# Performance work log

Hardware: AMD Instinct MI355X
Metric: run time of the kernel (lower is better)

## Reference

```python
import jax, jax.numpy as jnp
import numpy as np

DN = ('NCHW', 'HWIO', 'NCHW')  # NCHW data, HWIO kernels


def conv3x3(x, k, b=None):
    # 'same'-padded 3x3 conv, stride 1, NCHW layout
    y = jax.lax.conv_general_dilated(x, k, (1, 1), 'SAME', dimension_numbers=DN)
    if b is not None:
        y = y + b[None, :, None, None]
    return y


def setup_inputs() -> dict:
    B, T, C, H, W = 4, 4, 256, 30, 40
    CA = 256  # nb_filters_att (== nb_filters_out == nb_filters_in per SAM)
    key = jax.random.key(0)
    ks = jax.random.split(key, 10)
    s = 0.05  # small init scale so gates don't saturate
    x = jax.random.normal(ks[0], (B, T, C, H, W), dtype=jnp.float32)
    # attention convs
    Wa = jax.random.normal(ks[1], (3, 3, C, CA), dtype=jnp.float32) * s
    ba = jnp.zeros((CA,), dtype=jnp.float32)
    Ua = jax.random.normal(ks[2], (3, 3, C, CA), dtype=jnp.float32) * s
    bua = jnp.zeros((CA,), dtype=jnp.float32)
    # V_a has attentive_init='zero' in the original; random here for a nontrivial baseline
    Va = jax.random.normal(ks[3], (3, 3, CA, 1), dtype=jnp.float32) * s
    # gate convs: stack i,f,c,o along output channels (same math as 4 separate 3x3 convs)
    Wx = jax.random.normal(ks[4], (3, 3, C, 4 * C), dtype=jnp.float32) * s
    bx = jnp.zeros((4 * C,), dtype=jnp.float32)
    Uh = jax.random.normal(ks[5], (3, 3, C, 4 * C), dtype=jnp.float32) * s
    bh = jnp.zeros((4 * C,), dtype=jnp.float32)
    return {"x": x, "Wa": Wa, "ba": ba, "Ua": Ua, "bua": bua, "Va": Va,
            "Wx": Wx, "bx": bx, "Uh": Uh, "bh": bh}


def reference(x, Wa, ba, Ua, bua, Va, Wx, bx, Uh, bh):
    B, T, C, H, W = x.shape
    # initial h and c: sum over the time axis (K.sum(x, axis=1))
    h0 = jnp.sum(x, axis=1)
    c0 = h0

    def step(carry, xt):
        h, c = carry
        # conv-based spatial attention
        e = conv3x3(jnp.tanh(conv3x3(h, Wa, ba) + conv3x3(xt, Ua, bua)), Va)  # [B,1,H,W]
        a = jax.nn.softmax(e.reshape(B, -1), axis=-1).reshape(B, 1, H, W)
        x_tilde = xt * a  # broadcast over channels
        # fused gate convs: i | f | c | o along channel axis
        g = conv3x3(x_tilde, Wx, bx) + conv3x3(h, Uh, bh)  # [B,4C,H,W]
        gi, gf, gc, go = jnp.split(g, 4, axis=1)
        i = jax.nn.sigmoid(gi)
        f = jax.nn.sigmoid(gf)
        o = jax.nn.sigmoid(go)
        c_new = f * c + i * jnp.tanh(gc)
        h_new = o * jnp.tanh(c_new)
        return (h_new, c_new), None

    (h_last, _), _ = jax.lax.scan(step, (h0, c0), jnp.swapaxes(x, 0, 1))
    return h_last  # [B, C_out, H, W], the last RNN output
```

## Files before the change

### kernel.cpp

```cpp
#include <hip/hip_runtime.h>
#include <math.h>

#define BB 4
#define TT 4
#define CC 256
#define HH 30
#define WW 40
#define HWS (HH*WW)
#define CHW (CC*HWS)

typedef __attribute__((ext_vector_type(8))) _Float16 half8;
typedef __attribute__((ext_vector_type(4))) float f32x4;

__global__ void init_hc(const float* __restrict__ x,
                        float* __restrict__ h, float* __restrict__ c) {
    int id = blockIdx.x * 256 + threadIdx.x;
    if (id >= BB * CHW) return;
    int b = id / CHW;
    int rem = id - b * CHW;
    float s = 0.f;
#pragma unroll
    for (int t = 0; t < TT; ++t)
        s += x[((size_t)b * TT + t) * CHW + rem];
    h[id] = s;
    c[id] = s;
}

__global__ void pack_weights(const float* __restrict__ W1,
                             const float* __restrict__ W2,
                             _Float16* __restrict__ wt, int Cout) {
    int idx = blockIdx.x * 256 + threadIdx.x;
    if (idx >= 4608 * Cout) return;
    int k = idx / Cout;
    int n = idx - k * Cout;
    float v = (k < 2304) ? W1[(size_t)k * Cout + n]
                         : W2[(size_t)(k - 2304) * Cout + n];
    wt[((size_t)(k >> 3) * Cout + n) * 8 + (k & 7)] = (_Float16)v;
}

template<int NW>
__global__ __launch_bounds__(256) void conv_mfma(
    const float* __restrict__ in0, long bs0, const float* __restrict__ scale,
    const float* __restrict__ in1, long bs1,
    const _Float16* __restrict__ wt,
    const float* __restrict__ b1, const float* __restrict__ b2,
    float* __restrict__ out, int Cout)
{
    __shared__ alignas(16) _Float16 s_a[4 * 168 * 8];

    const int tid = threadIdx.x;
    const int l = tid & 63, wv = tid >> 6;
    const int q = l >> 4, r = l & 15;
    const int mb = blockIdx.x;
    const int b = mb / 15;
    const int pix0 = (mb % 15) * 80;
    const int y0 = (mb % 15) * 2;
    const int n0 = blockIdx.y * (4 * NW * 16) + wv * (NW * 16);
    const int z = blockIdx.z;

    const float* inp = z ? (in1 + (size_t)b * bs1) : (in0 + (size_t)b * bs0);
    const float* scl = z ? nullptr : scale;

    f32x4 acc[5][NW];
#pragma unroll
    for (int nt = 0; nt < NW; ++nt) {
        int co = n0 + nt * 16 + r;
        float bias = z ? 0.f : (b1[co] + b2[co]);
        f32x4 bv = {bias, bias, bias, bias};
#pragma unroll
        for (int mt = 0; mt < 5; ++mt) acc[mt][nt] = bv;
    }

    for (int ci0 = 0; ci0 < CC; ci0 += 32) {
        __syncthreads();
        for (int i = tid; i < 672; i += 256) {
            int cig = i / 168;
            int pix = i - cig * 168;
            int row = pix / 42;
            int px = pix - row * 42;
            int xx = px - 1, yy = y0 + row - 1;
            half8 hv = {0, 0, 0, 0, 0, 0, 0, 0};
            if (xx >= 0 && xx < WW && yy >= 0 && yy < HH) {
                const float* p0 = inp + (size_t)(ci0 + cig * 8) * HWS + yy * WW + xx;
                float sc = scl ? scl[(size_t)b * HWS + yy * WW + xx] : 1.f;
#pragma unroll
                for (int j = 0; j < 8; ++j)
                    hv[j] = (_Float16)(p0[(size_t)j * HWS] * sc);
            }
            *(half8*)&s_a[(cig * 168 + pix) * 8] = hv;
        }
        __syncthreads();

        const int kgb = z * 288 + (ci0 >> 3);
#pragma unroll
        for (int tap = 0; tap < 9; ++tap) {
            const int dy = tap / 3, dx = tap - dy * 3;
            const int kg = kgb + tap * 32 + q;
            half8 bf[NW];
#pragma unroll
            for (int nt = 0; nt < NW; ++nt) {
                size_t off = (size_t)kg * Cout + (n0 + nt * 16 + r);
                bf[nt] = ((const half8*)wt)[off];
            }
#pragma unroll
            for (int mt = 0; mt < 5; ++mt) {
                int p = mt * 16 + r;
                int ry = p / 40, rx = p - ry * 40;
                int hpix = (ry + dy) * 42 + rx + dx;
                half8 af = *(const half8*)&s_a[(q * 168 + hpix) * 8];
#pragma unroll
                for (int nt = 0; nt < NW; ++nt)
                    acc[mt][nt] = __builtin_amdgcn_mfma_f32_16x16x32_f16(
                        af, bf[nt], acc[mt][nt], 0, 0, 0);
            }
        }
    }

    out += (size_t)z * BB * Cout * HWS;
#pragma unroll
    for (int mt = 0; mt < 5; ++mt) {
#pragma unroll
        for (int nt = 0; nt < NW; ++nt) {
            int co = n0 + nt * 16 + r;
            int p = pix0 + mt * 16 + q * 4;
            *(f32x4*)&out[((size_t)b * Cout + co) * HWS + p] = acc[mt][nt];
        }
    }
}

__global__ void add_tanh(const float* __restrict__ a0, const float* __restrict__ a1,
                         float* __restrict__ o, int n) {
    int id = blockIdx.x * 256 + threadIdx.x;
    if (id < n) o[id] = tanhf(a0[id] + a1[id]);
}

__global__ __launch_bounds__(256) void att_e_part(
    const float* __restrict__ att, const float* __restrict__ Va,
    float* __restrict__ part)
{
    __shared__ float red[4][64];
    const int lane = threadIdx.x & 63, wv = threadIdx.x >> 6;
    const int p = blockIdx.x * 64 + lane;
    const int b = blockIdx.y, ch = blockIdx.z;
    const bool valid = (p < HWS);
    const int pc = valid ? p : 0;
    const int y = pc / WW, x = pc - (pc / WW) * WW;

    float acc = 0.f;
    if (valid) {
        const int ca0 = ch * 32 + wv * 8;
#pragma unroll
        for (int j = 0; j < 8; ++j) {
            const int ca = ca0 + j;
            const float* base = att + ((size_t)b * CC + ca) * HWS;
            const float* va = Va + ca;
#pragma unroll
            for (int dy = 0; dy < 3; ++dy) {
                int yy = y + dy - 1;
                if (yy < 0 || yy >= HH) continue;
#pragma unroll
                for (int dx = 0; dx < 3; ++dx) {
                    int xx = x + dx - 1;
                    if (xx < 0 || xx >= WW) continue;
                    acc = fmaf(base[yy * WW + xx], va[(dy * 3 + dx) * CC], acc);
                }
            }
        }
    }
    red[wv][lane] = acc;
    __syncthreads();
    if (wv == 0 && valid)
        part[((size_t)b * 8 + ch) * HWS + p] =
            red[0][lane] + red[1][lane] + red[2][lane] + red[3][lane];
}

__global__ __launch_bounds__(256) void softmax_kernel(
    const float* __restrict__ part, float* __restrict__ a)
{
    __shared__ float se[HWS];
    __shared__ float red[256];
    int b = blockIdx.x;
    int tid = threadIdx.x;

    for (int i = tid; i < HWS; i += 256) {
        float s = 0.f;
#pragma unroll
        for (int ch = 0; ch < 8; ++ch)
            s += part[((size_t)b * 8 + ch) * HWS + i];
        se[i] = s;
    }
    __syncthreads();

    float m = -1e30f;
    for (int i = tid; i < HWS; i += 256) m = fmaxf(m, se[i]);
    red[tid] = m;
    __syncthreads();
    for (int s = 128; s > 0; s >>= 1) {
        if (tid < s) red[tid] = fmaxf(red[tid], red[tid + s]);
        __syncthreads();
    }
    m = red[0];
    __syncthreads();

    float sum = 0.f;
    for (int i = tid; i < HWS; i += 256) {
        float v = expf(se[i] - m);
        se[i] = v;
        sum += v;
    }
    red[tid] = sum;
    __syncthreads();
    for (int s = 128; s > 0; s >>= 1) {
        if (tid < s) red[tid] += red[tid + s];
        __syncthreads();
    }
    float inv = 1.f / red[0];
    for (int i = tid; i < HWS; i += 256)
        a[(size_t)b * HWS + i] = se[i] * inv;
}

__global__ void gate_update(const float* __restrict__ g0, const float* __restrict__ g1,
                            float* __restrict__ c, float* __restrict__ h_out) {
    int id = blockIdx.x * 256 + threadIdx.x;
    if (id >= BB * CHW) return;
    int b = id / CHW;
    int rem = id - b * CHW;
    size_t gbase = (size_t)b * 4 * CHW + rem;
    float gi = g0[gbase] + g1[gbase];
    float gf = g0[gbase + CHW] + g1[gbase + CHW];
    float gc = g0[gbase + 2 * (size_t)CHW] + g1[gbase + 2 * (size_t)CHW];
    float go = g0[gbase + 3 * (size_t)CHW] + g1[gbase + 3 * (size_t)CHW];
    float i_ = 1.f / (1.f + expf(-gi));
    float f_ = 1.f / (1.f + expf(-gf));
    float o_ = 1.f / (1.f + expf(-go));
    float cn = f_ * c[id] + i_ * tanhf(gc);
    c[id] = cn;
    h_out[id] = o_ * tanhf(cn);
}

extern "C" void kernel_launch(void* const* d_in, const int* in_sizes, int n_in,
                              void* d_out, int out_size, void* d_ws, size_t ws_size,
                              hipStream_t stream) {
    const float* x   = (const float*)d_in[0];
    const float* Wa  = (const float*)d_in[1];
    const float* ba  = (const float*)d_in[2];
    const float* Ua  = (const float*)d_in[3];
    const float* bua = (const float*)d_in[4];
    const float* Va  = (const float*)d_in[5];
    const float* Wx  = (const float*)d_in[6];
    const float* bx  = (const float*)d_in[7];
    const float* Uh  = (const float*)d_in[8];
    const float* bh  = (const float*)d_in[9];
    float* out = (float*)d_out;

    char* wsb = (char*)d_ws;
    const size_t NCHW = (size_t)BB * CHW;
    _Float16* wtg = (_Float16*)wsb;               wsb += (size_t)4608 * 1024 * 2;
    _Float16* wta = (_Float16*)wsb;               wsb += (size_t)4608 * 256 * 2;
    float* h0   = (float*)wsb;                    wsb += NCHW * 4;
    float* h1   = (float*)wsb;                    wsb += NCHW * 4;
    float* cb   = (float*)wsb;                    wsb += NCHW * 4;
    float* att01= (float*)wsb;                    wsb += 2 * NCHW * 4;
    float* att  = (float*)wsb;                    wsb += NCHW * 4;
    float* g01  = (float*)wsb;                    wsb += 8 * NCHW * 4;
    float* part = (float*)wsb;                    wsb += (size_t)BB * 8 * HWS * 4;
    float* a    = (float*)wsb;

    pack_weights<<<dim3((4608 * 1024 + 255) / 256), dim3(256), 0, stream>>>(
        Wx, Uh, wtg, 1024);
    pack_weights<<<dim3((4608 * 256 + 255) / 256), dim3(256), 0, stream>>>(
        Wa, Ua, wta, 256);

    const int n = (int)NCHW;
    init_hc<<<dim3((n + 255) / 256), dim3(256), 0, stream>>>(x, h0, cb);

    float* hbuf[2] = {h0, h1};
    const long XT_BS = (long)TT * CHW;
    const long H_BS  = (long)CHW;

    for (int t = 0; t < TT; ++t) {
        const float* xt = x + (size_t)t * CHW;
        float* hcur = hbuf[t & 1];
        float* hnext = (t == TT - 1) ? out : hbuf[(t + 1) & 1];

        conv_mfma<1><<<dim3(60, 4, 2), dim3(256), 0, stream>>>(
            hcur, H_BS, nullptr, xt, XT_BS, wta, ba, bua, att01, 256);
        add_tanh<<<dim3((n + 255) / 256), dim3(256), 0, stream>>>(
            att01, att01 + NCHW, att, n);

        att_e_part<<<dim3(19, BB, 8), dim3(256), 0, stream>>>(att, Va, part);
        softmax_kernel<<<dim3(BB), dim3(256), 0, stream>>>(part, a);

        conv_mfma<2><<<dim3(60, 8, 2), dim3(256), 0, stream>>>(
            xt, XT_BS, a, hcur, H_BS, wtg, bx, bh, g01, 1024);

        gate_update<<<dim3((n + 255) / 256), dim3(256), 0, stream>>>(
            g01, g01 + 4 * NCHW, cb, hnext);
    }
}
```

Baseline: 658.3 us.

## Double-buffer conv staging, software-pipeline weight loads, split-K attention conv, vectorize elementwise

The MFMA conv kernel now double-buffers its shared-memory input tile. It prefetches the next channel chunk into registers while the current taps compute, and rotates weight registers so global weight loads overlap the MFMAs, with s_setprio raised around the compute. The attention conv is split over input channels, giving four partial outputs that add_tanh4 sums, so more blocks run on the small 256-output conv. init_hc, add_tanh and gate_update use float4 vector accesses. The changes add register pressure (launch bounds of 3 blocks per CU), double the shared memory, and write more partial-sum traffic in exchange for better latency hiding and parallelism.

```diff
diff --git a/kernel.cpp b/kernel.cpp
--- a/kernel.cpp
+++ b/kernel.cpp
@@ -8,6 +8,7 @@
 #define WW 40
 #define HWS (HH*WW)
 #define CHW (CC*HWS)
+#define CHW4 (CHW/4)
 
 typedef __attribute__((ext_vector_type(8))) _Float16 half8;
 typedef __attribute__((ext_vector_type(4))) float f32x4;
@@ -15,15 +16,16 @@
 __global__ void init_hc(const float* __restrict__ x,
                         float* __restrict__ h, float* __restrict__ c) {
     int id = blockIdx.x * 256 + threadIdx.x;
-    if (id >= BB * CHW) return;
-    int b = id / CHW;
-    int rem = id - b * CHW;
-    float s = 0.f;
+    if (id >= BB * CHW4) return;
+    int b = id / CHW4;
+    int rem = id - b * CHW4;
+    const f32x4* xv = (const f32x4*)x;
+    f32x4 s = {0.f, 0.f, 0.f, 0.f};
 #pragma unroll
     for (int t = 0; t < TT; ++t)
-        s += x[((size_t)b * TT + t) * CHW + rem];
-    h[id] = s;
-    c[id] = s;
+        s += xv[((size_t)b * TT + t) * CHW4 + rem];
+    ((f32x4*)h)[id] = s;
+    ((f32x4*)c)[id] = s;
 }
 
 __global__ void pack_weights(const float* __restrict__ W1,
@@ -38,15 +40,16 @@
     wt[((size_t)(k >> 3) * Cout + n) * 8 + (k & 7)] = (_Float16)v;
 }
 
-template<int NW>
-__global__ __launch_bounds__(256) void conv_mfma(
+template<int NW, int NZ>
+__global__ __launch_bounds__(256, 3) void conv_mfma(
     const float* __restrict__ in0, long bs0, const float* __restrict__ scale,
     const float* __restrict__ in1, long bs1,
     const _Float16* __restrict__ wt,
     const float* __restrict__ b1, const float* __restrict__ b2,
     float* __restrict__ out, int Cout)
 {
-    __shared__ alignas(16) _Float16 s_a[4 * 168 * 8];
+    constexpr int NK = 8 / NZ;
+    __shared__ alignas(16) _Float16 s_a[2][4 * 168 * 8];
 
     const int tid = threadIdx.x;
     const int l = tid & 63, wv = tid >> 6;
@@ -57,64 +60,124 @@
     const int y0 = (mb % 15) * 2;
     const int n0 = blockIdx.y * (4 * NW * 16) + wv * (NW * 16);
     const int z = blockIdx.z;
-
-    const float* inp = z ? (in1 + (size_t)b * bs1) : (in0 + (size_t)b * bs0);
-    const float* scl = z ? nullptr : scale;
+    const int src = z / NZ;
+    const int ci_start = (z % NZ) * (CC / NZ);
+    const int kgb0 = src * 288 + (ci_start >> 3);
+
+    const float* inp = (src ? in1 + (size_t)b * bs1 : in0 + (size_t)b * bs0)
+                       + (size_t)ci_start * HWS;
+    const float* scl = (src == 0) ? scale : nullptr;
+
+    bool iv[3], pv[3];
+    const float* pj[3];
+    float sc[3];
+    int ldsoff[3];
+#pragma unroll
+    for (int j = 0; j < 3; ++j) {
+        int item = tid + j * 256;
+        iv[j] = item < 672;
+        int it = iv[j] ? item : 0;
+        int cig = it / 168;
+        int pix = it - cig * 168;
+        int row = pix / 42;
+        int px = pix - row * 42;
+        int xx = px - 1, yy = y0 + row - 1;
+        pv[j] = iv[j] && xx >= 0 && xx < WW && yy >= 0 && yy < HH;
+        pj[j] = inp + (size_t)(cig * 8) * HWS + yy * WW + xx;
+        sc[j] = 1.f;
+        if (scl && pv[j]) sc[j] = scl[(size_t)b * HWS + yy * WW + xx];
+        ldsoff[j] = (cig * 168 + pix) * 8;
+    }
 
     f32x4 acc[5][NW];
 #pragma unroll
     for (int nt = 0; nt < NW; ++nt) {
         int co = n0 + nt * 16 + r;
-        float bias = z ? 0.f : (b1[co] + b2[co]);
+        float bias = (z == 0) ? (b1[co] + b2[co]) : 0.f;
         f32x4 bv = {bias, bias, bias, bias};
 #pragma unroll
         for (int mt = 0; mt < 5; ++mt) acc[mt][nt] = bv;
     }
 
-    for (int ci0 = 0; ci0 < CC; ci0 += 32) {
+    int hbase[5];
+#pragma unroll
+    for (int mt = 0; mt < 5; ++mt) {
+        int p = mt * 16 + r;
+        int ry = p / 40;
+        int rx = p - ry * 40;
+        hbase[mt] = ry * 42 + rx;
+    }
+
+    float sr[3][8];
+    auto stage_issue = [&](int kk) {
+#pragma unroll
+        for (int j = 0; j < 3; ++j) if (pv[j]) {
+            const float* p0 = pj[j] + (size_t)kk * 32 * HWS;
+#pragma unroll
+            for (int t = 0; t < 8; ++t) sr[j][t] = p0[(size_t)t * HWS];
+        }
+    };
+    auto stage_write = [&](int kk) {
+#pragma unroll
+        for (int j = 0; j < 3; ++j) if (iv[j]) {
+            half8 hv = {0, 0, 0, 0, 0, 0, 0, 0};
+            if (pv[j]) {
+#pragma unroll
+                for (int t = 0; t < 8; ++t)
+                    hv[t] = (_Float16)(sr[j][t] * sc[j]);
+            }
+            *(half8*)&s_a[kk & 1][ldsoff[j]] = hv;
+        }
+    };
+
+    const half8* wp = (const half8*)wt;
+    half8 w0[NW], w1[NW], w2[NW], w3[NW];
+
+#define WLOAD(SLOT, TAP) do {                                              \
+    const int kg_ = kgb0 + k * 4 + (TAP) * 32 + q;                         \
+    _Pragma("unroll")                                                      \
+    for (int nt = 0; nt < NW; ++nt)                                        \
+        SLOT[nt] = wp[(size_t)kg_ * Cout + n0 + nt * 16 + r];              \
+} while (0)
+
+#define CTAP(SLOT, TAP) do {                                               \
+    constexpr int dy_ = (TAP) / 3, dx_ = (TAP) % 3;                        \
+    _Pragma("unroll")                                                      \
+    for (int mt = 0; mt < 5; ++mt) {                                       \
+        half8 af = *(const half8*)&s_a[k & 1]                              \
+            [(q * 168 + hbase[mt] + dy_ * 42 + dx_) * 8];                  \
+        _Pragma("unroll")                                                  \
+        for (int nt = 0; nt < NW; ++nt)                                    \
+            acc[mt][nt] = __builtin_amdgcn_mfma_f32_16x16x32_f16(          \
+                af, SLOT[nt], acc[mt][nt], 0, 0, 0);                       \
+    }                                                                      \
+} while (0)
+
+    stage_issue(0);
+    stage_write(0);
+
+#pragma unroll
+    for (int k = 0; k < NK; ++k) {
+        WLOAD(w0, 0); WLOAD(w1, 1); WLOAD(w2, 2);
+        if (k + 1 < NK) stage_issue(k + 1);
         __syncthreads();
-        for (int i = tid; i < 672; i += 256) {
-            int cig = i / 168;
-            int pix = i - cig * 168;
-            int row = pix / 42;
-            int px = pix - row * 42;
-            int xx = px - 1, yy = y0 + row - 1;
-            half8 hv = {0, 0, 0, 0, 0, 0, 0, 0};
-            if (xx >= 0 && xx < WW && yy >= 0 && yy < HH) {
-                const float* p0 = inp + (size_t)(ci0 + cig * 8) * HWS + yy * WW + xx;
-                float sc = scl ? scl[(size_t)b * HWS + yy * WW + xx] : 1.f;
-#pragma unroll
-                for (int j = 0; j < 8; ++j)
-                    hv[j] = (_Float16)(p0[(size_t)j * HWS] * sc);
-            }
-            *(half8*)&s_a[(cig * 168 + pix) * 8] = hv;
-        }
-        __syncthreads();
-
-        const int kgb = z * 288 + (ci0 >> 3);
-#pragma unroll
-        for (int tap = 0; tap < 9; ++tap) {
-            const int dy = tap / 3, dx = tap - dy * 3;
-            const int kg = kgb + tap * 32 + q;
-            half8 bf[NW];
-#pragma unroll
-            for (int nt = 0; nt < NW; ++nt) {
-                size_t off = (size_t)kg * Cout + (n0 + nt * 16 + r);
-                bf[nt] = ((const half8*)wt)[off];
-            }
-#pragma unroll
-            for (int mt = 0; mt < 5; ++mt) {
-                int p = mt * 16 + r;
-                int ry = p / 40, rx = p - ry * 40;
-                int hpix = (ry + dy) * 42 + rx + dx;
-                half8 af = *(const half8*)&s_a[(q * 168 + hpix) * 8];
-#pragma unroll
-                for (int nt = 0; nt < NW; ++nt)
-                    acc[mt][nt] = __builtin_amdgcn_mfma_f32_16x16x32_f16(
-                        af, bf[nt], acc[mt][nt], 0, 0, 0);
-            }
-        }
-    }
+        __builtin_amdgcn_s_setprio(1);
+        WLOAD(w3, 3); CTAP(w0, 0);
+        WLOAD(w0, 4); CTAP(w1, 1);
+        WLOAD(w1, 5); CTAP(w2, 2);
+        WLOAD(w2, 6); CTAP(w3, 3);
+        WLOAD(w3, 7); CTAP(w0, 4);
+        WLOAD(w0, 8); CTAP(w1, 5);
+        __builtin_amdgcn_s_setprio(0);
+        if (k + 1 < NK) stage_write(k + 1);
+        __builtin_amdgcn_s_setprio(1);
+        CTAP(w2, 6);
+        CTAP(w3, 7);
+        CTAP(w0, 8);
+        __builtin_amdgcn_s_setprio(0);
+    }
+#undef WLOAD
+#undef CTAP
 
     out += (size_t)z * BB * Cout * HWS;
 #pragma unroll
@@ -128,10 +191,17 @@
     }
 }
 
-__global__ void add_tanh(const float* __restrict__ a0, const float* __restrict__ a1,
-                         float* __restrict__ o, int n) {
+__global__ void add_tanh4(const float* __restrict__ a0,
+                          float* __restrict__ o, int n4) {
     int id = blockIdx.x * 256 + threadIdx.x;
-    if (id < n) o[id] = tanhf(a0[id] + a1[id]);
+    if (id >= n4) return;
+    const f32x4* av = (const f32x4*)a0;
+    f32x4 s = av[id] + av[id + (size_t)n4] + av[id + 2 * (size_t)n4]
+            + av[id + 3 * (size_t)n4];
+    f32x4 rr;
+#pragma unroll
+    for (int j = 0; j < 4; ++j) rr[j] = tanhf(s[j]);
+    ((f32x4*)o)[id] = rr;
 }
 
 __global__ __launch_bounds__(256) void att_e_part(
@@ -222,20 +292,29 @@
 __global__ void gate_update(const float* __restrict__ g0, const float* __restrict__ g1,
                             float* __restrict__ c, float* __restrict__ h_out) {
     int id = blockIdx.x * 256 + threadIdx.x;
-    if (id >= BB * CHW) return;
-    int b = id / CHW;
-    int rem = id - b * CHW;
-    size_t gbase = (size_t)b * 4 * CHW + rem;
-    float gi = g0[gbase] + g1[gbase];
-    float gf = g0[gbase + CHW] + g1[gbase + CHW];
-    float gc = g0[gbase + 2 * (size_t)CHW] + g1[gbase + 2 * (size_t)CHW];
-    float go = g0[gbase + 3 * (size_t)CHW] + g1[gbase + 3 * (size_t)CHW];
-    float i_ = 1.f / (1.f + expf(-gi));
-    float f_ = 1.f / (1.f + expf(-gf));
-    float o_ = 1.f / (1.f + expf(-go));
-    float cn = f_ * c[id] + i_ * tanhf(gc);
-    c[id] = cn;
-    h_out[id] = o_ * tanhf(cn);
+    if (id >= BB * CHW4) return;
+    int b = id / CHW4;
+    int rem = id - b * CHW4;
+    const f32x4* g0v = (const f32x4*)g0;
+    const f32x4* g1v = (const f32x4*)g1;
+    size_t gb = (size_t)b * 4 * CHW4 + rem;
+    f32x4 gi = g0v[gb] + g1v[gb];
+    f32x4 gf = g0v[gb + CHW4] + g1v[gb + CHW4];
+    f32x4 gc = g0v[gb + 2 * (size_t)CHW4] + g1v[gb + 2 * (size_t)CHW4];
+    f32x4 go = g0v[gb + 3 * (size_t)CHW4] + g1v[gb + 3 * (size_t)CHW4];
+    f32x4 cv = ((const f32x4*)c)[id];
+    f32x4 cn, hn;
+#pragma unroll
+    for (int j = 0; j < 4; ++j) {
+        float i_ = 1.f / (1.f + expf(-gi[j]));
+        float f_ = 1.f / (1.f + expf(-gf[j]));
+        float o_ = 1.f / (1.f + expf(-go[j]));
+        float cc = f_ * cv[j] + i_ * tanhf(gc[j]);
+        cn[j] = cc;
+        hn[j] = o_ * tanhf(cc);
+    }
+    ((f32x4*)c)[id] = cn;
+    ((f32x4*)h_out)[id] = hn;
 }
 
 extern "C" void kernel_launch(void* const* d_in, const int* in_sizes, int n_in,
@@ -260,19 +339,19 @@
     float* h0   = (float*)wsb;                    wsb += NCHW * 4;
     float* h1   = (float*)wsb;                    wsb += NCHW * 4;
     float* cb   = (float*)wsb;                    wsb += NCHW * 4;
-    float* att01= (float*)wsb;                    wsb += 2 * NCHW * 4;
+    float* g01  = (float*)wsb;                    wsb += 8 * NCHW * 4;
     float* att  = (float*)wsb;                    wsb += NCHW * 4;
-    float* g01  = (float*)wsb;                    wsb += 8 * NCHW * 4;
     float* part = (float*)wsb;                    wsb += (size_t)BB * 8 * HWS * 4;
     float* a    = (float*)wsb;
+    float* att01 = g01;
 
     pack_weights<<<dim3((4608 * 1024 + 255) / 256), dim3(256), 0, stream>>>(
         Wx, Uh, wtg, 1024);
     pack_weights<<<dim3((4608 * 256 + 255) / 256), dim3(256), 0, stream>>>(
         Wa, Ua, wta, 256);
 
-    const int n = (int)NCHW;
-    init_hc<<<dim3((n + 255) / 256), dim3(256), 0, stream>>>(x, h0, cb);
+    const int n4 = BB * CHW4;
+    init_hc<<<dim3((n4 + 255) / 256), dim3(256), 0, stream>>>(x, h0, cb);
 
     float* hbuf[2] = {h0, h1};
     const long XT_BS = (long)TT * CHW;
@@ -283,18 +362,18 @@
         float* hcur = hbuf[t & 1];
         float* hnext = (t == TT - 1) ? out : hbuf[(t + 1) & 1];
 
-        conv_mfma<1><<<dim3(60, 4, 2), dim3(256), 0, stream>>>(
+        conv_mfma<1, 2><<<dim3(60, 4, 4), dim3(256), 0, stream>>>(
             hcur, H_BS, nullptr, xt, XT_BS, wta, ba, bua, att01, 256);
-        add_tanh<<<dim3((n + 255) / 256), dim3(256), 0, stream>>>(
-            att01, att01 + NCHW, att, n);
+        add_tanh4<<<dim3((n4 + 255) / 256), dim3(256), 0, stream>>>(
+            att01, att, n4);
 
         att_e_part<<<dim3(19, BB, 8), dim3(256), 0, stream>>>(att, Va, part);
         softmax_kernel<<<dim3(BB), dim3(256), 0, stream>>>(part, a);
 
-        conv_mfma<2><<<dim3(60, 8, 2), dim3(256), 0, stream>>>(
+        conv_mfma<2, 1><<<dim3(60, 8, 2), dim3(256), 0, stream>>>(
             xt, XT_BS, a, hcur, H_BS, wtg, bx, bh, g01, 1024);
 
-        gate_update<<<dim3((n + 255) / 256), dim3(256), 0, stream>>>(
+        gate_update<<<dim3((n4 + 255) / 256), dim3(256), 0, stream>>>(
             g01, g01 + 4 * NCHW, cb, hnext);
     }
 }
```

Result: faster. 596.8 us (-9.3%).
